# Performance work log

Hardware: AMD Instinct MI355X
Metric: run time of the kernel (lower is better)

Reference implementation:

```python
import jax, jax.numpy as jnp
import numpy as np

G, P, D, K, H = 256, 1024, 128, 16, 32  # graphs, nodes/graph, feat dim, clusters, MLP hidden
N = G * P


def setup_inputs() -> dict:
    key = jax.random.key(0)
    k0, k1, k2 = jax.random.split(key, 3)
    node_feats = jax.random.normal(k0, (N, D), dtype=jnp.float32)
    W1 = jax.random.normal(k1, (D, H), dtype=jnp.float32) * (1.0 / np.sqrt(D))
    b1 = jnp.zeros((H,), dtype=jnp.float32)
    W2 = jax.random.normal(k2, (H, K), dtype=jnp.float32) * (1.0 / np.sqrt(H))
    b2 = jnp.zeros((K,), dtype=jnp.float32)
    n_node = jnp.full((G,), P, dtype=jnp.int32)
    return {"node_feats": node_feats, "W1": W1, "b1": b1, "W2": W2, "b2": b2, "n_node": n_node}


def reference(node_feats, W1, b1, W2, b2, n_node):
    num_nodes = node_feats.shape[0]
    num_graphs = n_node.shape[0]
    num_clusters = W2.shape[1]

    # MLP([32, K]) assignment logits + softmax
    h = jax.nn.relu(node_feats @ W1 + b1)
    assignments = jax.nn.softmax(h @ W2 + b2, axis=-1)  # [N, K]

    # graph id per node
    batch_indices = jnp.repeat(jnp.arange(num_graphs), n_node, total_repeat_length=num_nodes)

    # per-cluster weighted segment_sum (loop over small fixed K, as in the original)
    coarse = [
        jax.ops.segment_sum(node_feats * assignments[:, k:k + 1], batch_indices, num_segments=num_graphs)
        for k in range(num_clusters)
    ]
    coarse_nodes = jnp.stack(coarse, axis=1).reshape(-1, node_feats.shape[-1])  # [G*K, D]

    # fully-connected coarse edges per graph (nonzero of ones is row-major: sender repeated, receiver tiled)
    single_senders = jnp.repeat(jnp.arange(num_clusters), num_clusters)
    single_receivers = jnp.tile(jnp.arange(num_clusters), num_clusters)
    batch_offset = jnp.arange(num_graphs)[:, None] * num_clusters
    c_senders = (single_senders[None, :] + batch_offset).reshape(-1)
    c_receivers = (single_receivers[None, :] + batch_offset).reshape(-1)
    c_edges = jnp.ones((c_senders.shape[0], 1), dtype=node_feats.dtype)

    return coarse_nodes, assignments, c_senders, c_receivers, c_edges
```

## Files before the change

### kernel.cpp

```cpp
#include <hip/hip_runtime.h>
#include <hip/hip_bf16.h>
#include <cstdint>

#define G_ 256
#define P_ 1024
#define D_ 128
#define K_ 16
#define H_ 32
#define N_ (G_ * P_)

constexpr size_t OFF_COARSE = 0;
constexpr size_t OFF_ASSIGN = (size_t)G_ * K_ * D_;
constexpr size_t OFF_SEND   = OFF_ASSIGN + (size_t)N_ * K_;
constexpr size_t OFF_RECV   = OFF_SEND + (size_t)G_ * K_ * K_;
constexpr size_t OFF_EDGE   = OFF_RECV + (size_t)G_ * K_ * K_;

typedef __attribute__((ext_vector_type(8))) short bf16x8;
typedef __attribute__((ext_vector_type(4))) float f32x4;

__device__ __forceinline__ void splitf(float x, short& h, short& l) {
    const unsigned u = __float_as_uint(x);
    h = (short)(u >> 16);
    const float hf = __uint_as_float(u & 0xffff0000u);
    const float r = x - hf;
    l = (short)(__float_as_uint(r) >> 16);
}

__global__ __launch_bounds__(256, 3) void mlp_assign_mfma(
    const float* __restrict__ x, const float* __restrict__ W1,
    const float* __restrict__ b1, const float* __restrict__ W2,
    const float* __restrict__ b2, float* __restrict__ assign_out)
{
    __shared__ float    xstage[4][2048];
    __shared__ unsigned hstage[4][512];

    const int tid  = threadIdx.x;
    const int lane = tid & 63;
    const int wave = tid >> 6;
    const int q = lane >> 4;
    const int c = lane & 15;

    bf16x8 w1h[4][2], w1l[4][2];
#pragma unroll
    for (int kb = 0; kb < 4; ++kb)
#pragma unroll
        for (int nt = 0; nt < 2; ++nt)
#pragma unroll
            for (int e = 0; e < 8; ++e) {
                short hb, lb;
                splitf(W1[(kb * 32 + q * 8 + e) * H_ + nt * 16 + c], hb, lb);
                w1h[kb][nt][e] = hb; w1l[kb][nt][e] = lb;
            }
    bf16x8 w2h, w2l;
#pragma unroll
    for (int e = 0; e < 8; ++e) {
        short hb, lb;
        splitf(W2[(q * 8 + e) * K_ + c], hb, lb);
        w2h[e] = hb; w2l[e] = lb;
    }
    const float b1v0 = b1[c];
    const float b1v1 = b1[16 + c];
    const float b2v  = b2[c];

    float* xw = xstage[wave];
    unsigned* hw = hstage[wave];
    const size_t nodebase = (size_t)blockIdx.x * 256 + (size_t)wave * 64;

    float4 ld[8];
    {
        const float4* src = (const float4*)(x + nodebase * D_);
#pragma unroll
        for (int i = 0; i < 8; ++i) ld[i] = src[i * 64 + lane];
    }

#pragma unroll
    for (int mt = 0; mt < 4; ++mt) {
#pragma unroll
        for (int i = 0; i < 8; ++i) {
            const int cid  = i * 64 + lane;
            const int row  = cid >> 5;
            const int colf = (cid & 31) * 4;
            const int kb   = colf >> 5;
            const int win  = colf & 31;
            const int addr = (kb * 2048 + row * 128 + win * 4) ^ ((row & 7) << 4);
            *(float4*)((char*)xw + addr) = ld[i];
        }

        if (mt < 3) {
            const float4* src = (const float4*)(x + (nodebase + (size_t)(mt + 1) * 16) * D_);
#pragma unroll
            for (int i = 0; i < 8; ++i) ld[i] = src[i * 64 + lane];
        }

        f32x4 acc0 = {b1v0, b1v0, b1v0, b1v0};
        f32x4 acc1 = {b1v1, b1v1, b1v1, b1v1};
#pragma unroll
        for (int kb = 0; kb < 4; ++kb) {
            const int rb = kb * 2048 + c * 128 + q * 32;
            const int sw = (c & 7) << 4;
            const float4 v0 = *(const float4*)((char*)xw + (rb ^ sw));
            const float4 v1 = *(const float4*)((char*)xw + ((rb + 16) ^ sw));
            const float vv[8] = {v0.x, v0.y, v0.z, v0.w, v1.x, v1.y, v1.z, v1.w};
            bf16x8 ah, al;
#pragma unroll
            for (int e = 0; e < 8; ++e) {
                short hb, lb; splitf(vv[e], hb, lb);
                ah[e] = hb; al[e] = lb;
            }
            acc0 = __builtin_amdgcn_mfma_f32_16x16x32_bf16(ah, w1h[kb][0], acc0, 0, 0, 0);
            acc0 = __builtin_amdgcn_mfma_f32_16x16x32_bf16(ah, w1l[kb][0], acc0, 0, 0, 0);
            acc0 = __builtin_amdgcn_mfma_f32_16x16x32_bf16(al, w1h[kb][0], acc0, 0, 0, 0);
            acc1 = __builtin_amdgcn_mfma_f32_16x16x32_bf16(ah, w1h[kb][1], acc1, 0, 0, 0);
            acc1 = __builtin_amdgcn_mfma_f32_16x16x32_bf16(ah, w1l[kb][1], acc1, 0, 0, 0);
            acc1 = __builtin_amdgcn_mfma_f32_16x16x32_bf16(al, w1h[kb][1], acc1, 0, 0, 0);
        }

#pragma unroll
        for (int r = 0; r < 4; ++r) {
            const int row = q * 4 + r;
            const int xsw = (row & 7) << 2;
            short hb, lb;
            const float t0 = fmaxf(acc0[r], 0.f);
            splitf(t0, hb, lb);
            hw[(row * 32 + c) ^ xsw] =
                ((unsigned)(unsigned short)hb << 16) | (unsigned short)lb;
            const float t1 = fmaxf(acc1[r], 0.f);
            splitf(t1, hb, lb);
            hw[(row * 32 + 16 + c) ^ xsw] =
                ((unsigned)(unsigned short)hb << 16) | (unsigned short)lb;
        }

        const int hsw = (c & 7) << 2;
        const uint4 u0 = *(const uint4*)&hw[(c * 32 + q * 8) ^ hsw];
        const uint4 u1 = *(const uint4*)&hw[(c * 32 + q * 8 + 4) ^ hsw];
        const unsigned uu[8] = {u0.x, u0.y, u0.z, u0.w, u1.x, u1.y, u1.z, u1.w};
        bf16x8 ha, la;
#pragma unroll
        for (int e = 0; e < 8; ++e) {
            ha[e] = (short)(uu[e] >> 16);
            la[e] = (short)(uu[e] & 0xffffu);
        }
        f32x4 lacc = {b2v, b2v, b2v, b2v};
        lacc = __builtin_amdgcn_mfma_f32_16x16x32_bf16(ha, w2h, lacc, 0, 0, 0);
        lacc = __builtin_amdgcn_mfma_f32_16x16x32_bf16(ha, w2l, lacc, 0, 0, 0);
        lacc = __builtin_amdgcn_mfma_f32_16x16x32_bf16(la, w2h, lacc, 0, 0, 0);

#pragma unroll
        for (int r = 0; r < 4; ++r) {
            const float v = lacc[r];
            float mx = v;
#pragma unroll
            for (int s = 1; s < 16; s <<= 1) mx = fmaxf(mx, __shfl_xor(mx, s, 16));
            const float e = __expf(v - mx);
            float sum = e;
#pragma unroll
            for (int s = 1; s < 16; s <<= 1) sum += __shfl_xor(sum, s, 16);
            assign_out[(nodebase + (size_t)mt * 16 + q * 4 + r) * K_ + c] = e / sum;
        }
    }
}

#define FMA4(dst, v, sc)                                                      \
    dst.x = fmaf(v.x, sc, dst.x); dst.y = fmaf(v.y, sc, dst.y);               \
    dst.z = fmaf(v.z, sc, dst.z); dst.w = fmaf(v.w, sc, dst.w)

__global__ __launch_bounds__(1024, 4) void coarse_kernel(
    const float* __restrict__ x, const float* __restrict__ assign,
    const int* __restrict__ n_node, float* __restrict__ out)
{
    __shared__ float xs[2][32 * 128];
    __shared__ float as_[2][32 * 16];
    __shared__ int pref[G_];

    const int tid = threadIdx.x;
    const int g = blockIdx.x;

    if (tid < 256) {
        const int e = g * 256 + tid;
        out[OFF_SEND + e] = (float)(g * K_ + (tid >> 4));
        out[OFF_RECV + e] = (float)(g * K_ + (tid & 15));
        out[OFF_EDGE + e] = 1.0f;
    }

    if (tid < G_) pref[tid] = n_node[tid];
    __syncthreads();
    for (int st = 1; st < G_; st <<= 1) {
        int v = 0;
        if (tid < G_ && tid >= st) v = pref[tid - st];
        __syncthreads();
        if (tid < G_ && tid >= st) pref[tid] += v;
        __syncthreads();
    }
    const int start = (g == 0) ? 0 : min(pref[g - 1], N_);
    const int end   = (g == G_ - 1) ? N_ : min(pref[g], N_);

    const int dq = tid & 31;
    const int s  = tid >> 5;

    float4 acc[K_];
#pragma unroll
    for (int k = 0; k < K_; ++k) acc[k] = make_float4(0.f, 0.f, 0.f, 0.f);

    const int total = end - start;
    const int nfull = total >> 5;
    const int tail  = total & 31;

    float4 rx = make_float4(0.f, 0.f, 0.f, 0.f);
    float4 ra = make_float4(0.f, 0.f, 0.f, 0.f);
    if (nfull > 0) {
        rx = *(const float4*)(x + (size_t)start * D_ + tid * 4);
        if (tid < 128)
            ra = *(const float4*)(assign + (size_t)start * K_ + tid * 4);
    }

    int b = 0;
    for (int cc = 0; cc < nfull; ++cc) {
        *(float4*)(&xs[b][tid * 4]) = rx;
        if (tid < 128) *(float4*)(&as_[b][tid * 4]) = ra;
        __syncthreads();

        if (cc + 1 < nfull) {
            const size_t nb = (size_t)start + (size_t)(cc + 1) * 32;
            rx = *(const float4*)(x + nb * D_ + tid * 4);
            if (tid < 128)
                ra = *(const float4*)(assign + nb * K_ + tid * 4);
        }

        const float4 xv = *(const float4*)(&xs[b][s * D_ + dq * 4]);
        const float4* av = (const float4*)(&as_[b][s * K_]);
#pragma unroll
        for (int qq = 0; qq < 4; ++qq) {
            const float4 a = av[qq];
            FMA4(acc[4 * qq + 0], xv, a.x);
            FMA4(acc[4 * qq + 1], xv, a.y);
            FMA4(acc[4 * qq + 2], xv, a.z);
            FMA4(acc[4 * qq + 3], xv, a.w);
        }
        b ^= 1;
    }

    if (tail > 0 && s < tail) {
        const size_t n = (size_t)start + (size_t)nfull * 32 + s;
        const float4 xv = *(const float4*)(x + n * D_ + dq * 4);
        const float4* av = (const float4*)(assign + n * K_);
#pragma unroll
        for (int qq = 0; qq < 4; ++qq) {
            const float4 a = av[qq];
            FMA4(acc[4 * qq + 0], xv, a.x);
            FMA4(acc[4 * qq + 1], xv, a.y);
            FMA4(acc[4 * qq + 2], xv, a.z);
            FMA4(acc[4 * qq + 3], xv, a.w);
        }
    }

    __syncthreads();
    float* red = &xs[0][0];
#pragma unroll
    for (int k = 0; k < K_; ++k) {
        *(float4*)(&red[s * D_ + dq * 4]) = acc[k];
        __syncthreads();
        if (tid < D_) {
            float sum = 0.f;
#pragma unroll
            for (int ss = 0; ss < 32; ++ss) sum += red[ss * D_ + tid];
            out[OFF_COARSE + ((size_t)g * K_ + k) * D_ + tid] = sum;
        }
        __syncthreads();
    }
}

extern "C" void kernel_launch(void* const* d_in, const int* in_sizes, int n_in,
                              void* d_out, int out_size, void* d_ws, size_t ws_size,
                              hipStream_t stream)
{
    const float* x      = (const float*)d_in[0];
    const float* W1     = (const float*)d_in[1];
    const float* b1     = (const float*)d_in[2];
    const float* W2     = (const float*)d_in[3];
    const float* b2     = (const float*)d_in[4];
    const int*   n_node = (const int*)d_in[5];
    float* out = (float*)d_out;

    mlp_assign_mfma<<<N_ / 256, 256, 0, stream>>>(x, W1, b1, W2, b2, out + OFF_ASSIGN);
    coarse_kernel<<<G_, 1024, 0, stream>>>(x, out + OFF_ASSIGN, n_node, out);
}
```

Baseline: 78.83 us.

## Load x directly into MFMA fragments and move split weights to LDS

```diff
diff --git a/kernel.cpp b/kernel.cpp
--- a/kernel.cpp
+++ b/kernel.cpp
@@ -26,12 +26,13 @@
     l = (short)(__float_as_uint(r) >> 16);
 }
 
-__global__ __launch_bounds__(256, 3) void mlp_assign_mfma(
+__global__ __launch_bounds__(256, 4) void mlp_assign_mfma(
     const float* __restrict__ x, const float* __restrict__ W1,
     const float* __restrict__ b1, const float* __restrict__ W2,
     const float* __restrict__ b2, float* __restrict__ assign_out)
 {
-    __shared__ float    xstage[4][2048];
+    __shared__ short w1hi[4096], w1lo[4096];
+    __shared__ short w2hi[512],  w2lo[512];
     __shared__ unsigned hstage[4][512];
 
     const int tid  = threadIdx.x;
@@ -40,124 +41,127 @@
     const int q = lane >> 4;
     const int c = lane & 15;
 
-    bf16x8 w1h[4][2], w1l[4][2];
-#pragma unroll
-    for (int kb = 0; kb < 4; ++kb)
-#pragma unroll
-        for (int nt = 0; nt < 2; ++nt)
-#pragma unroll
-            for (int e = 0; e < 8; ++e) {
-                short hb, lb;
-                splitf(W1[(kb * 32 + q * 8 + e) * H_ + nt * 16 + c], hb, lb);
-                w1h[kb][nt][e] = hb; w1l[kb][nt][e] = lb;
-            }
-    bf16x8 w2h, w2l;
-#pragma unroll
-    for (int e = 0; e < 8; ++e) {
+    for (int i = tid; i < 4096; i += 256) {
+        const int e  = i & 7;
+        const int cc = (i >> 3) & 15;
+        const int qq = (i >> 7) & 3;
+        const int nt = (i >> 9) & 1;
+        const int kb = (i >> 10) & 3;
         short hb, lb;
-        splitf(W2[(q * 8 + e) * K_ + c], hb, lb);
-        w2h[e] = hb; w2l[e] = lb;
-    }
+        splitf(W1[(kb * 32 + qq * 8 + e) * H_ + nt * 16 + cc], hb, lb);
+        const int pos = (((kb * 2 + nt) * 4 + qq) * 16 + cc) * 8 + e;
+        w1hi[pos] = hb; w1lo[pos] = lb;
+    }
+    for (int i = tid; i < 512; i += 256) {
+        const int e  = i & 7;
+        const int cc = (i >> 3) & 15;
+        const int qq = (i >> 7) & 3;
+        short hb, lb;
+        splitf(W2[(qq * 8 + e) * K_ + cc], hb, lb);
+        const int pos = (qq * 16 + cc) * 8 + e;
+        w2hi[pos] = hb; w2lo[pos] = lb;
+    }
+    __syncthreads();
+
     const float b1v0 = b1[c];
     const float b1v1 = b1[16 + c];
     const float b2v  = b2[c];
 
-    float* xw = xstage[wave];
     unsigned* hw = hstage[wave];
     const size_t nodebase = (size_t)blockIdx.x * 256 + (size_t)wave * 64;
 
-    float4 ld[8];
-    {
-        const float4* src = (const float4*)(x + nodebase * D_);
-#pragma unroll
-        for (int i = 0; i < 8; ++i) ld[i] = src[i * 64 + lane];
-    }
-
-#pragma unroll
-    for (int mt = 0; mt < 4; ++mt) {
-#pragma unroll
-        for (int i = 0; i < 8; ++i) {
-            const int cid  = i * 64 + lane;
-            const int row  = cid >> 5;
-            const int colf = (cid & 31) * 4;
-            const int kb   = colf >> 5;
-            const int win  = colf & 31;
-            const int addr = (kb * 2048 + row * 128 + win * 4) ^ ((row & 7) << 4);
-            *(float4*)((char*)xw + addr) = ld[i];
-        }
-
-        if (mt < 3) {
-            const float4* src = (const float4*)(x + (nodebase + (size_t)(mt + 1) * 16) * D_);
-#pragma unroll
-            for (int i = 0; i < 8; ++i) ld[i] = src[i * 64 + lane];
-        }
-
-        f32x4 acc0 = {b1v0, b1v0, b1v0, b1v0};
-        f32x4 acc1 = {b1v1, b1v1, b1v1, b1v1};
-#pragma unroll
-        for (int kb = 0; kb < 4; ++kb) {
-            const int rb = kb * 2048 + c * 128 + q * 32;
-            const int sw = (c & 7) << 4;
-            const float4 v0 = *(const float4*)((char*)xw + (rb ^ sw));
-            const float4 v1 = *(const float4*)((char*)xw + ((rb + 16) ^ sw));
-            const float vv[8] = {v0.x, v0.y, v0.z, v0.w, v1.x, v1.y, v1.z, v1.w};
-            bf16x8 ah, al;
-#pragma unroll
-            for (int e = 0; e < 8; ++e) {
-                short hb, lb; splitf(vv[e], hb, lb);
-                ah[e] = hb; al[e] = lb;
-            }
-            acc0 = __builtin_amdgcn_mfma_f32_16x16x32_bf16(ah, w1h[kb][0], acc0, 0, 0, 0);
-            acc0 = __builtin_amdgcn_mfma_f32_16x16x32_bf16(ah, w1l[kb][0], acc0, 0, 0, 0);
-            acc0 = __builtin_amdgcn_mfma_f32_16x16x32_bf16(al, w1h[kb][0], acc0, 0, 0, 0);
-            acc1 = __builtin_amdgcn_mfma_f32_16x16x32_bf16(ah, w1h[kb][1], acc1, 0, 0, 0);
-            acc1 = __builtin_amdgcn_mfma_f32_16x16x32_bf16(ah, w1l[kb][1], acc1, 0, 0, 0);
-            acc1 = __builtin_amdgcn_mfma_f32_16x16x32_bf16(al, w1h[kb][1], acc1, 0, 0, 0);
-        }
-
-#pragma unroll
-        for (int r = 0; r < 4; ++r) {
-            const int row = q * 4 + r;
-            const int xsw = (row & 7) << 2;
-            short hb, lb;
-            const float t0 = fmaxf(acc0[r], 0.f);
-            splitf(t0, hb, lb);
-            hw[(row * 32 + c) ^ xsw] =
-                ((unsigned)(unsigned short)hb << 16) | (unsigned short)lb;
-            const float t1 = fmaxf(acc1[r], 0.f);
-            splitf(t1, hb, lb);
-            hw[(row * 32 + 16 + c) ^ xsw] =
-                ((unsigned)(unsigned short)hb << 16) | (unsigned short)lb;
-        }
-
-        const int hsw = (c & 7) << 2;
-        const uint4 u0 = *(const uint4*)&hw[(c * 32 + q * 8) ^ hsw];
-        const uint4 u1 = *(const uint4*)&hw[(c * 32 + q * 8 + 4) ^ hsw];
-        const unsigned uu[8] = {u0.x, u0.y, u0.z, u0.w, u1.x, u1.y, u1.z, u1.w};
-        bf16x8 ha, la;
-#pragma unroll
-        for (int e = 0; e < 8; ++e) {
-            ha[e] = (short)(uu[e] >> 16);
-            la[e] = (short)(uu[e] & 0xffffu);
-        }
-        f32x4 lacc = {b2v, b2v, b2v, b2v};
-        lacc = __builtin_amdgcn_mfma_f32_16x16x32_bf16(ha, w2h, lacc, 0, 0, 0);
-        lacc = __builtin_amdgcn_mfma_f32_16x16x32_bf16(ha, w2l, lacc, 0, 0, 0);
-        lacc = __builtin_amdgcn_mfma_f32_16x16x32_bf16(la, w2h, lacc, 0, 0, 0);
-
-#pragma unroll
-        for (int r = 0; r < 4; ++r) {
-            const float v = lacc[r];
-            float mx = v;
-#pragma unroll
-            for (int s = 1; s < 16; s <<= 1) mx = fmaxf(mx, __shfl_xor(mx, s, 16));
-            const float e = __expf(v - mx);
-            float sum = e;
-#pragma unroll
-            for (int s = 1; s < 16; s <<= 1) sum += __shfl_xor(sum, s, 16);
-            assign_out[(nodebase + (size_t)mt * 16 + q * 4 + r) * K_ + c] = e / sum;
-        }
-    }
+#define LOAD_TILE(dst, mt)                                                    \
+    {                                                                         \
+        const float* rp = x + (nodebase + (size_t)(mt) * 16 + c) * D_ + q * 8;\
+        _Pragma("unroll")                                                     \
+        for (int kb = 0; kb < 4; ++kb) {                                      \
+            dst[kb * 2 + 0] = *(const float4*)(rp + kb * 32);                 \
+            dst[kb * 2 + 1] = *(const float4*)(rp + kb * 32 + 4);             \
+        }                                                                     \
+    }
+
+#define PROCESS_TILE(cur, nxt, mt, do_pref)                                   \
+    {                                                                         \
+        f32x4 acc0 = {b1v0, b1v0, b1v0, b1v0};                                \
+        f32x4 acc1 = {b1v1, b1v1, b1v1, b1v1};                                \
+        if (do_pref) LOAD_TILE(nxt, (mt) + 1);                                \
+        _Pragma("unroll")                                                     \
+        for (int kb = 0; kb < 4; ++kb) {                                      \
+            const float vv[8] = {cur[kb*2].x, cur[kb*2].y, cur[kb*2].z, cur[kb*2].w, \
+                                 cur[kb*2+1].x, cur[kb*2+1].y, cur[kb*2+1].z, cur[kb*2+1].w}; \
+            bf16x8 ah, al;                                                    \
+            _Pragma("unroll")                                                 \
+            for (int e = 0; e < 8; ++e) {                                     \
+                short hb, lb; splitf(vv[e], hb, lb);                          \
+                ah[e] = hb; al[e] = lb;                                       \
+            }                                                                 \
+            const bf16x8 bh0 = *(const bf16x8*)&w1hi[((kb * 2 + 0) * 4 + q) * 128 + c * 8]; \
+            const bf16x8 bl0 = *(const bf16x8*)&w1lo[((kb * 2 + 0) * 4 + q) * 128 + c * 8]; \
+            const bf16x8 bh1 = *(const bf16x8*)&w1hi[((kb * 2 + 1) * 4 + q) * 128 + c * 8]; \
+            const bf16x8 bl1 = *(const bf16x8*)&w1lo[((kb * 2 + 1) * 4 + q) * 128 + c * 8]; \
+            acc0 = __builtin_amdgcn_mfma_f32_16x16x32_bf16(ah, bh0, acc0, 0, 0, 0); \
+            acc0 = __builtin_amdgcn_mfma_f32_16x16x32_bf16(ah, bl0, acc0, 0, 0, 0); \
+            acc0 = __builtin_amdgcn_mfma_f32_16x16x32_bf16(al, bh0, acc0, 0, 0, 0); \
+            acc1 = __builtin_amdgcn_mfma_f32_16x16x32_bf16(ah, bh1, acc1, 0, 0, 0); \
+            acc1 = __builtin_amdgcn_mfma_f32_16x16x32_bf16(ah, bl1, acc1, 0, 0, 0); \
+            acc1 = __builtin_amdgcn_mfma_f32_16x16x32_bf16(al, bh1, acc1, 0, 0, 0); \
+        }                                                                     \
+                   \
+        _Pragma("unroll")                                                     \
+        for (int r = 0; r < 4; ++r) {                                         \
+            const int row = q * 4 + r;                                        \
+            const int xsw = (row & 7) << 2;                                   \
+            short hb, lb;                                                     \
+            splitf(fmaxf(acc0[r], 0.f), hb, lb);                              \
+            hw[(row * 32 + c) ^ xsw] =                                        \
+                ((unsigned)(unsigned short)hb << 16) | (unsigned short)lb;    \
+            splitf(fmaxf(acc1[r], 0.f), hb, lb);                              \
+            hw[(row * 32 + 16 + c) ^ xsw] =                                   \
+                ((unsigned)(unsigned short)hb << 16) | (unsigned short)lb;    \
+        }                                                                     \
+         \
+        {                                                                     \
+            const int hsw = (c & 7) << 2;                                     \
+            const uint4 u0 = *(const uint4*)&hw[(c * 32 + q * 8) ^ hsw];      \
+            const uint4 u1 = *(const uint4*)&hw[(c * 32 + q * 8 + 4) ^ hsw];  \
+            const unsigned uu[8] = {u0.x, u0.y, u0.z, u0.w, u1.x, u1.y, u1.z, u1.w}; \
+            bf16x8 ha, la;                                                    \
+            _Pragma("unroll")                                                 \
+            for (int e = 0; e < 8; ++e) {                                     \
+                ha[e] = (short)(uu[e] >> 16);                                 \
+                la[e] = (short)(uu[e] & 0xffffu);                             \
+            }                                                                 \
+            const bf16x8 wh = *(const bf16x8*)&w2hi[(q * 16 + c) * 8];        \
+            const bf16x8 wl = *(const bf16x8*)&w2lo[(q * 16 + c) * 8];        \
+            f32x4 lacc = {b2v, b2v, b2v, b2v};                                \
+            lacc = __builtin_amdgcn_mfma_f32_16x16x32_bf16(ha, wh, lacc, 0, 0, 0); \
+            lacc = __builtin_amdgcn_mfma_f32_16x16x32_bf16(ha, wl, lacc, 0, 0, 0); \
+            lacc = __builtin_amdgcn_mfma_f32_16x16x32_bf16(la, wh, lacc, 0, 0, 0); \
+                        \
+            _Pragma("unroll")                                                 \
+            for (int r = 0; r < 4; ++r) {                                     \
+                const float v = lacc[r];                                      \
+                float mx = v;                                                 \
+                _Pragma("unroll")                                             \
+                for (int s = 1; s < 16; s <<= 1) mx = fmaxf(mx, __shfl_xor(mx, s, 16)); \
+                const float ev = __expf(v - mx);                              \
+                float sum = ev;                                               \
+                _Pragma("unroll")                                             \
+                for (int s = 1; s < 16; s <<= 1) sum += __shfl_xor(sum, s, 16); \
+                assign_out[(nodebase + (size_t)(mt) * 16 + q * 4 + r) * K_ + c] = ev / sum; \
+            }                                                                 \
+        }                                                                     \
+    }
+
+    float4 ldA[8], ldB[8];
+    LOAD_TILE(ldA, 0);
+    PROCESS_TILE(ldA, ldB, 0, true);
+    PROCESS_TILE(ldB, ldA, 1, true);
+    PROCESS_TILE(ldA, ldB, 2, true);
+    PROCESS_TILE(ldB, ldA, 3, false);
+
+#undef LOAD_TILE
+#undef PROCESS_TILE
 }
 
 #define FMA4(dst, v, sc)                                                      \
```

Result: faster. 65.62 us (-16.8%).

## Use single-pass bf16 MFMA, direct fragment loads, and drop softmax max-subtraction

Applied to the files above, without the earlier changes.

```diff
diff --git a/kernel.cpp b/kernel.cpp
--- a/kernel.cpp
+++ b/kernel.cpp
@@ -18,20 +18,23 @@
 typedef __attribute__((ext_vector_type(8))) short bf16x8;
 typedef __attribute__((ext_vector_type(4))) float f32x4;
 
-__device__ __forceinline__ void splitf(float x, short& h, short& l) {
-    const unsigned u = __float_as_uint(x);
-    h = (short)(u >> 16);
-    const float hf = __uint_as_float(u & 0xffff0000u);
-    const float r = x - hf;
-    l = (short)(__float_as_uint(r) >> 16);
-}
-
-__global__ __launch_bounds__(256, 3) void mlp_assign_mfma(
+__device__ __forceinline__ unsigned rpack(float a, float b) {
+    const unsigned ua = __float_as_uint(a) + 0x8000u;
+    const unsigned ub = __float_as_uint(b) + 0x8000u;
+    return (ua >> 16) | (ub & 0xffff0000u);
+}
+__device__ __forceinline__ short rbf16(float a) {
+    return (short)((__float_as_uint(a) + 0x8000u) >> 16);
+}
+
+union FragU { uint4 u; bf16x8 v; };
+
+__global__ __launch_bounds__(256, 4) void mlp_assign_mfma(
     const float* __restrict__ x, const float* __restrict__ W1,
     const float* __restrict__ b1, const float* __restrict__ W2,
     const float* __restrict__ b2, float* __restrict__ assign_out)
 {
-    __shared__ float    xstage[4][2048];
+    __shared__ short    w1s[4096];
     __shared__ unsigned hstage[4][512];
 
     const int tid  = threadIdx.x;
@@ -40,123 +43,110 @@
     const int q = lane >> 4;
     const int c = lane & 15;
 
-    bf16x8 w1h[4][2], w1l[4][2];
-#pragma unroll
-    for (int kb = 0; kb < 4; ++kb)
-#pragma unroll
-        for (int nt = 0; nt < 2; ++nt)
-#pragma unroll
-            for (int e = 0; e < 8; ++e) {
-                short hb, lb;
-                splitf(W1[(kb * 32 + q * 8 + e) * H_ + nt * 16 + c], hb, lb);
-                w1h[kb][nt][e] = hb; w1l[kb][nt][e] = lb;
-            }
-    bf16x8 w2h, w2l;
-#pragma unroll
-    for (int e = 0; e < 8; ++e) {
-        short hb, lb;
-        splitf(W2[(q * 8 + e) * K_ + c], hb, lb);
-        w2h[e] = hb; w2l[e] = lb;
+    for (int i = tid; i < 4096; i += 256) {
+        const int e  = i & 7;
+        const int cc = (i >> 3) & 15;
+        const int qq = (i >> 7) & 3;
+        const int nt = (i >> 9) & 1;
+        const int kb = (i >> 10) & 3;
+        w1s[(((kb * 2 + nt) * 4 + qq) * 16 + cc) * 8 + e] =
+            rbf16(W1[(kb * 32 + qq * 8 + e) * H_ + nt * 16 + cc]);
+    }
+    __syncthreads();
+
+    FragU w2f;
+    {
+        float wv[8];
+#pragma unroll
+        for (int e = 0; e < 8; ++e) wv[e] = W2[(q * 8 + e) * K_ + c];
+        w2f.u = make_uint4(rpack(wv[0], wv[1]), rpack(wv[2], wv[3]),
+                           rpack(wv[4], wv[5]), rpack(wv[6], wv[7]));
     }
     const float b1v0 = b1[c];
     const float b1v1 = b1[16 + c];
     const float b2v  = b2[c];
 
-    float* xw = xstage[wave];
     unsigned* hw = hstage[wave];
     const size_t nodebase = (size_t)blockIdx.x * 256 + (size_t)wave * 64;
 
     float4 ld[8];
     {
-        const float4* src = (const float4*)(x + nodebase * D_);
-#pragma unroll
-        for (int i = 0; i < 8; ++i) ld[i] = src[i * 64 + lane];
+        const float* rp = x + (nodebase + c) * D_ + q * 8;
+#pragma unroll
+        for (int kb = 0; kb < 4; ++kb) {
+            ld[kb * 2 + 0] = *(const float4*)(rp + kb * 32);
+            ld[kb * 2 + 1] = *(const float4*)(rp + kb * 32 + 4);
+        }
     }
 
 #pragma unroll
     for (int mt = 0; mt < 4; ++mt) {
-#pragma unroll
-        for (int i = 0; i < 8; ++i) {
-            const int cid  = i * 64 + lane;
-            const int row  = cid >> 5;
-            const int colf = (cid & 31) * 4;
-            const int kb   = colf >> 5;
-            const int win  = colf & 31;
-            const int addr = (kb * 2048 + row * 128 + win * 4) ^ ((row & 7) << 4);
-            *(float4*)((char*)xw + addr) = ld[i];
-        }
-
+        FragU af[4];
+#pragma unroll
+        for (int kb = 0; kb < 4; ++kb) {
+            const float4 v0 = ld[kb * 2 + 0];
+            const float4 v1 = ld[kb * 2 + 1];
+            af[kb].u = make_uint4(rpack(v0.x, v0.y), rpack(v0.z, v0.w),
+                                  rpack(v1.x, v1.y), rpack(v1.z, v1.w));
+        }
         if (mt < 3) {
-            const float4* src = (const float4*)(x + (nodebase + (size_t)(mt + 1) * 16) * D_);
-#pragma unroll
-            for (int i = 0; i < 8; ++i) ld[i] = src[i * 64 + lane];
+            const float* rp = x + (nodebase + (size_t)(mt + 1) * 16 + c) * D_ + q * 8;
+#pragma unroll
+            for (int kb = 0; kb < 4; ++kb) {
+                ld[kb * 2 + 0] = *(const float4*)(rp + kb * 32);
+                ld[kb * 2 + 1] = *(const float4*)(rp + kb * 32 + 4);
+            }
         }
 
         f32x4 acc0 = {b1v0, b1v0, b1v0, b1v0};
         f32x4 acc1 = {b1v1, b1v1, b1v1, b1v1};
 #pragma unroll
         for (int kb = 0; kb < 4; ++kb) {
-            const int rb = kb * 2048 + c * 128 + q * 32;
-            const int sw = (c & 7) << 4;
-            const float4 v0 = *(const float4*)((char*)xw + (rb ^ sw));
-            const float4 v1 = *(const float4*)((char*)xw + ((rb + 16) ^ sw));
-            const float vv[8] = {v0.x, v0.y, v0.z, v0.w, v1.x, v1.y, v1.z, v1.w};
-            bf16x8 ah, al;
-#pragma unroll
-            for (int e = 0; e < 8; ++e) {
-                short hb, lb; splitf(vv[e], hb, lb);
-                ah[e] = hb; al[e] = lb;
-            }
-            acc0 = __builtin_amdgcn_mfma_f32_16x16x32_bf16(ah, w1h[kb][0], acc0, 0, 0, 0);
-            acc0 = __builtin_amdgcn_mfma_f32_16x16x32_bf16(ah, w1l[kb][0], acc0, 0, 0, 0);
-            acc0 = __builtin_amdgcn_mfma_f32_16x16x32_bf16(al, w1h[kb][0], acc0, 0, 0, 0);
-            acc1 = __builtin_amdgcn_mfma_f32_16x16x32_bf16(ah, w1h[kb][1], acc1, 0, 0, 0);
-            acc1 = __builtin_amdgcn_mfma_f32_16x16x32_bf16(ah, w1l[kb][1], acc1, 0, 0, 0);
-            acc1 = __builtin_amdgcn_mfma_f32_16x16x32_bf16(al, w1h[kb][1], acc1, 0, 0, 0);
+            const bf16x8 bh0 = *(const bf16x8*)&w1s[((kb * 2 + 0) * 4 + q) * 128 + c * 8];
+            const bf16x8 bh1 = *(const bf16x8*)&w1s[((kb * 2 + 1) * 4 + q) * 128 + c * 8];
+            acc0 = __builtin_amdgcn_mfma_f32_16x16x32_bf16(af[kb].v, bh0, acc0, 0, 0, 0);
+            acc1 = __builtin_amdgcn_mfma_f32_16x16x32_bf16(af[kb].v, bh1, acc1, 0, 0, 0);
         }
 
 #pragma unroll
         for (int r = 0; r < 4; ++r) {
             const int row = q * 4 + r;
             const int xsw = (row & 7) << 2;
-            short hb, lb;
-            const float t0 = fmaxf(acc0[r], 0.f);
-            splitf(t0, hb, lb);
             hw[(row * 32 + c) ^ xsw] =
-                ((unsigned)(unsigned short)hb << 16) | (unsigned short)lb;
-            const float t1 = fmaxf(acc1[r], 0.f);
-            splitf(t1, hb, lb);
+                (unsigned)(unsigned short)rbf16(fmaxf(acc0[r], 0.f));
             hw[(row * 32 + 16 + c) ^ xsw] =
-                ((unsigned)(unsigned short)hb << 16) | (unsigned short)lb;
+                (unsigned)(unsigned short)rbf16(fmaxf(acc1[r], 0.f));
         }
 
         const int hsw = (c & 7) << 2;
         const uint4 u0 = *(const uint4*)&hw[(c * 32 + q * 8) ^ hsw];
         const uint4 u1 = *(const uint4*)&hw[(c * 32 + q * 8 + 4) ^ hsw];
-        const unsigned uu[8] = {u0.x, u0.y, u0.z, u0.w, u1.x, u1.y, u1.z, u1.w};
-        bf16x8 ha, la;
-#pragma unroll
-        for (int e = 0; e < 8; ++e) {
-            ha[e] = (short)(uu[e] >> 16);
-            la[e] = (short)(uu[e] & 0xffffu);
-        }
+        FragU ha;
+        ha.u.x = (u0.x & 0xffffu) | (u0.y << 16);
+        ha.u.y = (u0.z & 0xffffu) | (u0.w << 16);
+        ha.u.z = (u1.x & 0xffffu) | (u1.y << 16);
+        ha.u.w = (u1.z & 0xffffu) | (u1.w << 16);
+
         f32x4 lacc = {b2v, b2v, b2v, b2v};
-        lacc = __builtin_amdgcn_mfma_f32_16x16x32_bf16(ha, w2h, lacc, 0, 0, 0);
-        lacc = __builtin_amdgcn_mfma_f32_16x16x32_bf16(ha, w2l, lacc, 0, 0, 0);
-        lacc = __builtin_amdgcn_mfma_f32_16x16x32_bf16(la, w2h, lacc, 0, 0, 0);
-
-#pragma unroll
-        for (int r = 0; r < 4; ++r) {
-            const float v = lacc[r];
-            float mx = v;
-#pragma unroll
-            for (int s = 1; s < 16; s <<= 1) mx = fmaxf(mx, __shfl_xor(mx, s, 16));
-            const float e = __expf(v - mx);
-            float sum = e;
-#pragma unroll
-            for (int s = 1; s < 16; s <<= 1) sum += __shfl_xor(sum, s, 16);
-            assign_out[(nodebase + (size_t)mt * 16 + q * 4 + r) * K_ + c] = e / sum;
-        }
+        lacc = __builtin_amdgcn_mfma_f32_16x16x32_bf16(ha.v, w2f.v, lacc, 0, 0, 0);
+
+        float ex0 = __expf(lacc[0]);
+        float ex1 = __expf(lacc[1]);
+        float ex2 = __expf(lacc[2]);
+        float ex3 = __expf(lacc[3]);
+        float s0 = ex0, s1 = ex1, s2 = ex2, s3 = ex3;
+#pragma unroll
+        for (int s = 1; s < 16; s <<= 1) {
+            s0 += __shfl_xor(s0, s, 16);
+            s1 += __shfl_xor(s1, s, 16);
+            s2 += __shfl_xor(s2, s, 16);
+            s3 += __shfl_xor(s3, s, 16);
+        }
+        const size_t ob = (nodebase + (size_t)mt * 16 + q * 4) * K_ + c;
+        assign_out[ob + 0 * K_] = ex0 / s0;
+        assign_out[ob + 1 * K_] = ex1 / s1;
+        assign_out[ob + 2 * K_] = ex2 / s2;
+        assign_out[ob + 3 * K_] = ex3 / s3;
     }
 }
 
```

Result: faster. 64.84 us (-17.7%).
